# Kernel optimization log

Hardware: AMD Instinct MI355X
Metric: run time of the kernel (lower is better)

The kernel has to match this reference:

```python
import jax, jax.numpy as jnp
from jax import lax
import numpy as np

B, CIN, COUT, N, H, W = 16, 64, 64, 8, 128, 128


def setup_inputs() -> dict:
    key = jax.random.key(0)
    ks = jax.random.split(key, 6)
    s = 0.05
    return {
        "x": jax.random.normal(ks[0], (B, CIN, H, W), dtype=jnp.float32),
        "condition": jax.random.normal(ks[1], (B, CIN), dtype=jnp.float32),
        "filt_w": jax.random.normal(ks[2], (N, COUT, CIN, 3, 3), dtype=jnp.float32) * s,
        "filt_b": jax.random.normal(ks[3], (N, COUT), dtype=jnp.float32) * s,
        "sel_w": jax.random.normal(ks[4], (N, CIN), dtype=jnp.float32) * s,
        "sel_b": jax.random.normal(ks[5], (N,), dtype=jnp.float32) * s,
    }


def reference(x, condition, filt_w, filt_b, sel_w, sel_b):
    b = x.shape[0]
    # condition selector: Linear(in_channels -> num_conditions) + softmax
    logits = condition.reshape(b, -1) @ sel_w.T + sel_b          # [B, N]
    weights = jax.nn.softmax(logits, axis=-1)                    # [B, N]

    n, cout, cin, kh, kw = filt_w.shape
    # Run all N branch convs in ONE conv by stacking filters on the output-channel axis.
    kern = filt_w.reshape(n * cout, cin, kh, kw)
    y = lax.conv_general_dilated(
        x, kern, window_strides=(1, 1), padding="SAME",
        dimension_numbers=("NCHW", "OIHW", "NCHW"))              # [B, N*COUT, H, W]
    h, w = y.shape[-2], y.shape[-1]
    y = y.reshape(b, n, cout, h, w) + filt_b.reshape(1, n, cout, 1, 1)
    # softmax-gated sum over the N branches
    out = jnp.einsum("bn,bnohw->bohw", weights, y)
    return out
```

## Files before the change

### kernel.cpp

```cpp
#include <hip/hip_runtime.h>
#include <stdint.h>

#define BATCH 16
#define CIN   64
#define COUT  64
#define NBR   8
#define HH    128
#define WW    128
#define XBH   130
#define XBW   130
#define PSTR  68
#define NTILES 1024

typedef __attribute__((ext_vector_type(8)))  short short8;
typedef __attribute__((ext_vector_type(16))) float f32x16;

__device__ __forceinline__ unsigned int f2bf_hi(float f) {
    union { float f; uint32_t u; } v; v.f = f;
    return (v.u + 0x8000u) >> 16;
}
__device__ __forceinline__ unsigned short f2bf(float f) {
    union { float f; uint32_t u; } v; v.f = f;
    uint32_t u = v.u;
    return (unsigned short)((u + 0x7FFFu + ((u >> 16) & 1u)) >> 16);
}
__device__ __forceinline__ short8 gld_frag(const unsigned short* p) {
    union { uint4 u; short8 s; } t;
    t.u = *(const uint4*)p;
    return t.s;
}
__device__ __forceinline__ short8 lds_frag(const unsigned short* p) {
    union { uint2 u[2]; short8 s; } t;
    t.u[0] = *(const uint2*)p;
    t.u[1] = *(const uint2*)(p + 4);
    return t.s;
}
__device__ __forceinline__ void gload_lds16(const unsigned short* g, unsigned short* l) {
    __builtin_amdgcn_global_load_lds(
        (const __attribute__((address_space(1))) unsigned int*)g,
        (__attribute__((address_space(3))) unsigned int*)l, 16, 0, 0);
}

__global__ __launch_bounds__(256)
void k_pc(const float* __restrict__ cond,
          const float* __restrict__ sel_w,
          const float* __restrict__ sel_b,
          const float* __restrict__ filt_w,
          const float* __restrict__ filt_b,
          const float* __restrict__ x,
          unsigned short* __restrict__ wfilt,
          float* __restrict__ cbias,
          unsigned short* __restrict__ xb) {
    __shared__ __align__(16) char smem[NBR * 144 * 16 + 64];
    const int tid = threadIdx.x;

    if (blockIdx.x < NTILES) {
        float4* lw4 = (float4*)smem;
        float*  lg  = (float*)(smem + NBR * 144 * 16);
        float*  lw  = (float*)lw4;
        const int blk = blockIdx.x;
        const int b = blk >> 6, o = blk & 63;

        const float4* src4 = (const float4*)filt_w;
        #pragma unroll
        for (int i = tid; i < NBR * 144; i += 256)
            lw4[i] = src4[((i / 144) * COUT + o) * 144 + (i % 144)];

        {
            const int lane = tid & 63, w = tid >> 6;
            const float c0 = cond[b * CIN + lane];
            #pragma unroll
            for (int k = 0; k < 2; ++k) {
                const int n = w + k * 4;
                float p = c0 * sel_w[n * CIN + lane];
                #pragma unroll
                for (int off = 32; off > 0; off >>= 1)
                    p += __shfl_down(p, off, 64);
                if (lane == 0) lg[n] = p + sel_b[n];
            }
        }
        __syncthreads();

        float w8[NBR];
        {
            float m = -1e30f;
            #pragma unroll
            for (int n = 0; n < NBR; ++n) m = fmaxf(m, lg[n]);
            float s = 0.f;
            #pragma unroll
            for (int n = 0; n < NBR; ++n) { w8[n] = __expf(lg[n] - m); s += w8[n]; }
            const float inv = 1.f / s;
            #pragma unroll
            for (int n = 0; n < NBR; ++n) w8[n] *= inv;
        }

        #pragma unroll
        for (int idx = tid; idx < 576; idx += 256) {
            const int t = idx >> 6, c = idx & 63;
            float acc = 0.f;
            #pragma unroll
            for (int n = 0; n < NBR; ++n)
                acc += w8[n] * lw[n * 576 + c * 9 + t];
            wfilt[(((long)(b * 9 + t) * COUT + o) << 6) + c] = f2bf(acc);
        }
        if (tid == 0) {
            float ab = 0.f;
            #pragma unroll
            for (int n = 0; n < NBR; ++n) ab += w8[n] * filt_b[n * COUT + o];
            cbias[b * COUT + o] = ab;
        }
    } else {
        const int id = blockIdx.x - NTILES;
        const int hp = id % XBH;
        const int b  = id / XBH;
        unsigned short* dst = xb + (long)(b * XBH + hp) * XBW * PSTR;

        if (hp == 0 || hp == XBH - 1) {
            uint2 z; z.x = z.y = 0u;
            for (int t = tid; t < XBW * PSTR / 4; t += 256)
                *(uint2*)&dst[t * 4] = z;
            return;
        }
        const int h = hp - 1;

        unsigned short* lt = (unsigned short*)smem;

        #pragma unroll
        for (int k = 0; k < 8; ++k) {
            const int u = tid + k * 256;
            const int c = u >> 5;
            const int j = u & 31;
            const float4 v = *(const float4*)(x + ((long)(b * CIN + c) * HH + h) * WW + j * 4);
            const int w = j * 4;
            lt[(w    ) * 66 + c] = (unsigned short)f2bf_hi(v.x);
            lt[(w + 1) * 66 + c] = (unsigned short)f2bf_hi(v.y);
            lt[(w + 2) * 66 + c] = (unsigned short)f2bf_hi(v.z);
            lt[(w + 3) * 66 + c] = (unsigned short)f2bf_hi(v.w);
        }
        __syncthreads();

        for (int t = tid; t < XBW * 8; t += 256) {
            const int wp = t >> 3, q = t & 7;
            uint2 u0, u1;
            u0.x = u0.y = u1.x = u1.y = 0u;
            if (wp > 0 && wp < XBW - 1) {
                const unsigned int* lp = (const unsigned int*)&lt[(wp - 1) * 66 + q * 8];
                u0.x = lp[0]; u0.y = lp[1]; u1.x = lp[2]; u1.y = lp[3];
            }
            unsigned short* dp = dst + wp * PSTR + q * 8;
            *(uint2*)dp       = u0;
            *(uint2*)(dp + 4) = u1;
            if (q == 7) {
                uint2 z; z.x = z.y = 0u;
                *(uint2*)(dst + wp * PSTR + 64) = z;
            }
        }
    }
}

#define RT 4
#define WT 32
#define SLABW 34
#define SLABR 6
#define ROWUS (SLABW * PSTR)
#define NCHUNK (SLABR * ROWUS / 8)

__global__ __launch_bounds__(256, 5)
void k_conv(const unsigned short* __restrict__ xb,
            const unsigned short* __restrict__ wfilt,
            const float* __restrict__ cbias,
            float* __restrict__ out) {
    __shared__ unsigned short lx[SLABR * ROWUS];

    const int b  = blockIdx.z;
    const int h0 = blockIdx.y * RT;
    const int w0 = blockIdx.x * WT;
    const int tid = threadIdx.x;

    const unsigned short* srcb = xb + ((long)(b * XBH + h0) * XBW + w0) * PSTR;
    #pragma unroll
    for (int k = 0; k < 7; ++k) {
        const int t = tid + k * 256;
        if (t < NCHUNK) {
            const int row = t / 289;
            const int rc  = t - row * 289;
            gload_lds16(srcb + (long)row * (XBW * PSTR) + rc * 8, lx + t * 8);
        }
    }

    const int lane = tid & 63;
    const int wave = tid >> 6;
    const int l31  = lane & 31;
    const int lh   = lane >> 5;
    const int wp   = wave & 1;
    const int wc   = wave >> 1;
    const int r0   = wp * 2;

    const unsigned short* wf = wfilt + (long)b * 9 * COUT * CIN + wc * 32 * CIN;

    short8 A[4];
    #pragma unroll
    for (int cc = 0; cc < 4; ++cc)
        A[cc] = gld_frag(wf + l31 * CIN + cc * 16 + lh * 8);

    f32x16 acc0, acc1;
    #pragma unroll
    for (int i = 0; i < 16; ++i) {
        const int m = (i & 3) + 8 * (i >> 2) + 4 * lh;
        const float bb = cbias[b * COUT + wc * 32 + m];
        acc0[i] = bb; acc1[i] = bb;
    }

    __syncthreads();

    #pragma unroll
    for (int tap = 0; tap < 9; ++tap) {
        short8 nA[4];
        if (tap < 8) {
            const unsigned short* wn = wf + (long)(tap + 1) * COUT * CIN;
            #pragma unroll
            for (int cc = 0; cc < 4; ++cc)
                nA[cc] = gld_frag(wn + l31 * CIN + cc * 16 + lh * 8);
        }
        const int kh = tap / 3, kw = tap % 3;
        #pragma unroll
        for (int cc = 0; cc < 4; ++cc) {
            const int kofs = cc * 16 + lh * 8;
            short8 b0 = lds_frag(&lx[((r0     + kh) * SLABW + l31 + kw) * PSTR + kofs]);
            short8 b1 = lds_frag(&lx[((r0 + 1 + kh) * SLABW + l31 + kw) * PSTR + kofs]);
            acc0 = __builtin_amdgcn_mfma_f32_32x32x16_bf16(A[cc], b0, acc0, 0, 0, 0);
            acc1 = __builtin_amdgcn_mfma_f32_32x32x16_bf16(A[cc], b1, acc1, 0, 0, 0);
        }
        #pragma unroll
        for (int cc = 0; cc < 4; ++cc) A[cc] = nA[cc];
    }

    #pragma unroll
    for (int pb = 0; pb < 2; ++pb) {
        const f32x16 v = pb == 0 ? acc0 : acc1;
        const int hrow = h0 + r0 + pb;
        float* op = out + (((long)(b * COUT + wc * 32) * HH + hrow) * WW + w0 + l31);
        #pragma unroll
        for (int i = 0; i < 16; ++i) {
            const int m = (i & 3) + 8 * (i >> 2) + 4 * lh;
            op[(long)m * HH * WW] = v[i];
        }
    }
}

extern "C" void kernel_launch(void* const* d_in, const int* in_sizes, int n_in,
                              void* d_out, int out_size, void* d_ws, size_t ws_size,
                              hipStream_t stream) {
    const float* x      = (const float*)d_in[0];
    const float* cond   = (const float*)d_in[1];
    const float* filt_w = (const float*)d_in[2];
    const float* filt_b = (const float*)d_in[3];
    const float* sel_w  = (const float*)d_in[4];
    const float* sel_b  = (const float*)d_in[5];
    float* out = (float*)d_out;

    float*          cbias = (float*)d_ws;
    unsigned short* wfilt = (unsigned short*)((char*)d_ws + 4096);
    unsigned short* xb    = (unsigned short*)((char*)d_ws + 4096 + 1179648);

    k_pc<<<NTILES + BATCH * XBH, 256, 0, stream>>>(cond, sel_w, sel_b, filt_w, filt_b, x,
                                                   wfilt, cbias, xb);

    dim3 grid(WW / WT, HH / RT, BATCH);
    k_conv<<<grid, 256, 0, stream>>>(xb, wfilt, cbias, out);
}
```

Measured before the change: 173.8 us.

## Halve conv row tile, remap workgroups across XCDs, raise occupancy

```diff
diff --git a/kernel.cpp b/kernel.cpp
--- a/kernel.cpp
+++ b/kernel.cpp
@@ -158,35 +158,29 @@
     }
 }
 
-#define RT 4
+#define RT 2
 #define WT 32
 #define SLABW 34
-#define SLABR 6
+#define SLABR 4
 #define ROWUS (SLABW * PSTR)
 #define NCHUNK (SLABR * ROWUS / 8)
-
-__global__ __launch_bounds__(256, 5)
+#define NWG    4096
+
+__global__ __launch_bounds__(256, 8)
 void k_conv(const unsigned short* __restrict__ xb,
             const unsigned short* __restrict__ wfilt,
             const float* __restrict__ cbias,
             float* __restrict__ out) {
     __shared__ unsigned short lx[SLABR * ROWUS];
 
-    const int b  = blockIdx.z;
-    const int h0 = blockIdx.y * RT;
-    const int w0 = blockIdx.x * WT;
+    const int orig = blockIdx.x;
+    const int wgid = (orig & 7) * (NWG / 8) + (orig >> 3);
+    const int tx = wgid & 3;
+    const int ty = (wgid >> 2) & 63;
+    const int b  = wgid >> 8;
+    const int h0 = ty * RT;
+    const int w0 = tx * WT;
     const int tid = threadIdx.x;
-
-    const unsigned short* srcb = xb + ((long)(b * XBH + h0) * XBW + w0) * PSTR;
-    #pragma unroll
-    for (int k = 0; k < 7; ++k) {
-        const int t = tid + k * 256;
-        if (t < NCHUNK) {
-            const int row = t / 289;
-            const int rc  = t - row * 289;
-            gload_lds16(srcb + (long)row * (XBW * PSTR) + rc * 8, lx + t * 8);
-        }
-    }
 
     const int lane = tid & 63;
     const int wave = tid >> 6;
@@ -194,22 +188,27 @@
     const int lh   = lane >> 5;
     const int wp   = wave & 1;
     const int wc   = wave >> 1;
-    const int r0   = wp * 2;
 
     const unsigned short* wf = wfilt + (long)b * 9 * COUT * CIN + wc * 32 * CIN;
-
     short8 A[4];
     #pragma unroll
     for (int cc = 0; cc < 4; ++cc)
         A[cc] = gld_frag(wf + l31 * CIN + cc * 16 + lh * 8);
 
-    f32x16 acc0, acc1;
-    #pragma unroll
-    for (int i = 0; i < 16; ++i) {
-        const int m = (i & 3) + 8 * (i >> 2) + 4 * lh;
-        const float bb = cbias[b * COUT + wc * 32 + m];
-        acc0[i] = bb; acc1[i] = bb;
-    }
+    const unsigned short* srcb = xb + ((long)(b * XBH + h0) * XBW + w0) * PSTR;
+    #pragma unroll
+    for (int k = 0; k < 5; ++k) {
+        const int t = tid + k * 256;
+        if (t < NCHUNK) {
+            const int row = t / 289;
+            const int rc  = t - row * 289;
+            gload_lds16(srcb + (long)row * (XBW * PSTR) + rc * 8, lx + t * 8);
+        }
+    }
+
+    f32x16 acc;
+    #pragma unroll
+    for (int i = 0; i < 16; ++i) acc[i] = 0.f;
 
     __syncthreads();
 
@@ -226,25 +225,19 @@
         #pragma unroll
         for (int cc = 0; cc < 4; ++cc) {
             const int kofs = cc * 16 + lh * 8;
-            short8 b0 = lds_frag(&lx[((r0     + kh) * SLABW + l31 + kw) * PSTR + kofs]);
-            short8 b1 = lds_frag(&lx[((r0 + 1 + kh) * SLABW + l31 + kw) * PSTR + kofs]);
-            acc0 = __builtin_amdgcn_mfma_f32_32x32x16_bf16(A[cc], b0, acc0, 0, 0, 0);
-            acc1 = __builtin_amdgcn_mfma_f32_32x32x16_bf16(A[cc], b1, acc1, 0, 0, 0);
+            short8 b0 = lds_frag(&lx[((wp + kh) * SLABW + l31 + kw) * PSTR + kofs]);
+            acc = __builtin_amdgcn_mfma_f32_32x32x16_bf16(A[cc], b0, acc, 0, 0, 0);
         }
         #pragma unroll
         for (int cc = 0; cc < 4; ++cc) A[cc] = nA[cc];
     }
 
-    #pragma unroll
-    for (int pb = 0; pb < 2; ++pb) {
-        const f32x16 v = pb == 0 ? acc0 : acc1;
-        const int hrow = h0 + r0 + pb;
-        float* op = out + (((long)(b * COUT + wc * 32) * HH + hrow) * WW + w0 + l31);
-        #pragma unroll
-        for (int i = 0; i < 16; ++i) {
-            const int m = (i & 3) + 8 * (i >> 2) + 4 * lh;
-            op[(long)m * HH * WW] = v[i];
-        }
+    const int hrow = h0 + wp;
+    float* op = out + (((long)(b * COUT + wc * 32) * HH + hrow) * WW + w0 + l31);
+    #pragma unroll
+    for (int i = 0; i < 16; ++i) {
+        const int m = (i & 3) + 8 * (i >> 2) + 4 * lh;
+        op[(long)m * HH * WW] = acc[i] + cbias[b * COUT + wc * 32 + m];
     }
 }
 
@@ -266,6 +259,5 @@
     k_pc<<<NTILES + BATCH * XBH, 256, 0, stream>>>(cond, sel_w, sel_b, filt_w, filt_b, x,
                                                    wfilt, cbias, xb);
 
-    dim3 grid(WW / WT, HH / RT, BATCH);
-    k_conv<<<grid, 256, 0, stream>>>(xb, wfilt, cbias, out);
-}
+    k_conv<<<NWG, 256, 0, stream>>>(xb, wfilt, cbias, out);
+}
```

Result: slower. 192.1 us (+10.6%).
